# Optimization experiments

Measured on AMD Instinct MI355X. Metric: run time of the kernel, lower is better.

## Reference

```python
import jax, jax.numpy as jnp
import numpy as np

N = 50000   # nodes
D = 128     # feature / out_channels
E = 800000  # edges per edge type
L = 2       # num_layers
T = 2       # num edge types


def setup_inputs() -> dict:
    key = jax.random.key(0)
    ks = jax.random.split(key, 6)
    x = jax.random.normal(ks[0], (N, D), dtype=jnp.float32)
    h = jax.random.normal(ks[1], (N, D), dtype=jnp.float32)  # unused by forward, kept for fidelity
    edge_index_a = jax.random.randint(ks[2], (2, E), 0, N)
    edge_index_b = jax.random.randint(ks[3], (2, E), 0, N)
    Wl = (jax.random.normal(ks[4], (L, T, D, D), dtype=jnp.float32) * 0.05)
    bl = jnp.zeros((L, T, D), dtype=jnp.float32)
    Wr = (jax.random.normal(ks[5], (L, T, D, D), dtype=jnp.float32) * 0.05)
    return {"x": x, "h": h, "edge_index_a": edge_index_a, "edge_index_b": edge_index_b,
            "Wl": Wl, "bl": bl, "Wr": Wr}


def _sage(x, edge_index, Wl, bl, Wr):
    # PyG SAGEConv: lin_l(mean_{j->i} x_j) + lin_r(x_i); lin_l has bias, lin_r does not.
    src, dst = edge_index[0], edge_index[1]
    msg_sum = jax.ops.segment_sum(x[src], dst, num_segments=N)            # [N, D]
    deg = jax.ops.segment_sum(jnp.ones((edge_index.shape[1],), x.dtype), dst, num_segments=N)
    mean = msg_sum / jnp.maximum(deg, 1.0)[:, None]
    return mean @ Wl + bl + x @ Wr


def reference(x, h, edge_index_a, edge_index_b, Wl, bl, Wr):
    out = x
    for l in range(L):
        # HeteroConv default aggregation: sum over edge types with same dst node type
        out = (_sage(out, edge_index_a, Wl[l, 0], bl[l, 0], Wr[l, 0])
               + _sage(out, edge_index_b, Wl[l, 1], bl[l, 1], Wr[l, 1]))
    return jax.nn.sigmoid(out)
```

## Files before the change

### kernel.cpp

```cpp
#include <hip/hip_runtime.h>
#include <math.h>

#define N_NODES 50000
#define D 128
#define NE 800000
#define BN 64
#define NBUCK 782
#define CAP 1280
#define EPB 4096
#define PBLK 196
#define F2B_BLKS 6250
#define WPREP_BLKS 384
#define MPITCH 68

typedef unsigned int uint;
typedef unsigned short ushort;
typedef unsigned char uchar;

using bf16x8 = __attribute__((ext_vector_type(8))) short;
using f32x4  = __attribute__((ext_vector_type(4))) float;

__device__ __forceinline__ float bflo(uint w) {
    union { uint u; float f; } c; c.u = w << 16; return c.f;
}
__device__ __forceinline__ float bfhi(uint w) {
    union { uint u; float f; } c; c.u = w & 0xffff0000u; return c.f;
}
__device__ __forceinline__ uint fp2bf_rn(float f) {
    union { float f; uint u; } c; c.f = f;
    return (c.u + 0x7fffu + ((c.u >> 16) & 1u)) >> 16;
}

__global__ __launch_bounds__(256) void build_kernel(
    const float4* __restrict__ x4, uint2* __restrict__ featb2,
    uint* __restrict__ feat8w,
    const float* __restrict__ Wl, const float* __restrict__ Wr,
    ushort* __restrict__ Wpack,
    const int* __restrict__ srcA, const int* __restrict__ dstA,
    const int* __restrict__ srcB, const int* __restrict__ dstB,
    int* __restrict__ bcurA, int* __restrict__ bcurB,
    uint* __restrict__ ebufA, uint* __restrict__ ebufB) {
    const int blk = blockIdx.x;
    const int t   = threadIdx.x;
    if (blk < 2 * PBLK) {
        __shared__ int h[NBUCK];
        __shared__ int base[NBUCK];
        const int typ = blk >= PBLK;
        const int* src = typ ? srcB : srcA;
        const int* dst = typ ? dstB : dstA;
        int* bc        = typ ? bcurB : bcurA;
        uint* ebuf     = typ ? ebufB : ebufA;
        const int e0 = (blk - (typ ? PBLK : 0)) * EPB;
        for (int j = t; j < NBUCK; j += 256) h[j] = 0;
        __syncthreads();
#pragma unroll
        for (int i = 0; i < EPB / 256; ++i) {
            const int e = e0 + t + i * 256;
            if (e < NE) atomicAdd(&h[dst[e] >> 6], 1);
        }
        __syncthreads();
        for (int j = t; j < NBUCK; j += 256) {
            const int c = h[j];
            base[j] = c ? atomicAdd(&bc[j], c) : 0;
            h[j] = 0;
        }
        __syncthreads();
#pragma unroll
        for (int i = 0; i < EPB / 256; ++i) {
            const int e = e0 + t + i * 256;
            if (e < NE) {
                const int d  = dst[e];
                const int bk = d >> 6;
                const int pos = atomicAdd(&h[bk], 1);
                const int off = base[bk] + pos;
                if (off < CAP)
                    ebuf[(size_t)bk * CAP + off] = (uint)src[e] | ((uint)(d & 63) << 17);
            }
        }
    } else if (blk < 2 * PBLK + F2B_BLKS) {
        const int i = (blk - 2 * PBLK) * 256 + t;
        float4 v = x4[i];
        uint2 o;
        o.x = fp2bf_rn(v.x) | (fp2bf_rn(v.y) << 16);
        o.y = fp2bf_rn(v.z) | (fp2bf_rn(v.w) << 16);
        featb2[i] = o;
        int pk = __builtin_amdgcn_cvt_pk_fp8_f32(v.x, v.y, 0, false);
        pk = __builtin_amdgcn_cvt_pk_fp8_f32(v.z, v.w, pk, true);
        feat8w[i] = (uint)pk;
    } else {
        const int i   = (blk - 2 * PBLK - F2B_BLKS) * 256 + t;
        const int l   = i / 49152;
        const int rem = i % 49152;
        const int ks  = rem / 4096;
        const int n   = (rem % 4096) / 32;
        const int kk  = rem % 32;
        const int r   = ks * 32 + kk;
        float v;
        if (r < 128)       v = Wl[(((size_t)l * 2 + 0) * 128 + r) * 128 + n];
        else if (r < 256)  v = Wl[(((size_t)l * 2 + 1) * 128 + (r - 128)) * 128 + n];
        else               v = Wr[(((size_t)l * 2 + 0) * 128 + (r - 256)) * 128 + n]
                             + Wr[(((size_t)l * 2 + 1) * 128 + (r - 256)) * 128 + n];
        Wpack[i] = (ushort)fp2bf_rn(v);
    }
}

__global__ __launch_bounds__(256) void csrfill_kernel(
    const uint* __restrict__ ebufA, const uint* __restrict__ ebufB,
    const int* __restrict__ bcntA, const int* __restrict__ bcntB,
    ushort* __restrict__ lidxA, ushort* __restrict__ lidxB,
    int* __restrict__ pbeg, int* __restrict__ pdeg, uchar* __restrict__ ord) {
    __shared__ uint rlds[2][CAP];
    __shared__ int cnt[128], ex[128], cur[128];
    const int b = blockIdx.x;
    const int t = threadIdx.x;

    if (t < 128) cnt[t] = 0;
    int countA = bcntA[b]; if (countA > CAP) countA = CAP;
    int countB = bcntB[b]; if (countB > CAP) countB = CAP;
    const uint* ebA = ebufA + (size_t)b * CAP;
    const uint* ebB = ebufB + (size_t)b * CAP;
    for (int e = t; e < countA; e += 256) rlds[0][e] = ebA[e];
    for (int e = t; e < countB; e += 256) rlds[1][e] = ebB[e];
    __syncthreads();
    for (int e = t; e < countA; e += 256) atomicAdd(&cnt[rlds[0][e] >> 17], 1);
    for (int e = t; e < countB; e += 256) atomicAdd(&cnt[64 + (rlds[1][e] >> 17)], 1);
    __syncthreads();
    if (t < 128) ex[t] = cnt[t];
    __syncthreads();
    for (int off = 1; off < 64; off <<= 1) {
        int v = 0;
        if (t < 128 && (t & 63) >= off) v = ex[t - off];
        __syncthreads();
        if (t < 128 && (t & 63) >= off) ex[t] += v;
        __syncthreads();
    }
    if (t < 128) {
        ex[t] -= cnt[t];
        cur[t] = ex[t];
        const int node = b * BN + (t & 63);
        if (node < N_NODES) {
            const int base = (t >> 6) * N_NODES;
            pbeg[base + node] = b * CAP + ex[t];
            pdeg[base + node] = cnt[t];
        }
        const int li = cnt[t];
        int r = 0;
#pragma unroll 8
        for (int j = 0; j < 128; ++j) {
            const int lj = cnt[j];
            r += (lj > li) || (lj == li && j < t);
        }
        ord[b * 128 + r] = (uchar)t;
    }
    __syncthreads();
    for (int e = t; e < countA; e += 256) {
        const uint rec = rlds[0][e];
        const int p = atomicAdd(&cur[rec >> 17], 1);
        lidxA[(size_t)b * CAP + p] = (ushort)(rec & 0x1FFFFu);
    }
    for (int e = t; e < countB; e += 256) {
        const uint rec = rlds[1][e];
        const int p = atomicAdd(&cur[64 + (rec >> 17)], 1);
        lidxB[(size_t)b * CAP + p] = (ushort)(rec & 0x1FFFFu);
    }
}

__global__ __launch_bounds__(1024, 8) void fused_kernel(
    const uint4* __restrict__ feat,
    const uint4* __restrict__ feat8,
    const ushort* __restrict__ lidxA, const ushort* __restrict__ lidxB,
    const int* __restrict__ pbeg, const int* __restrict__ pdeg,
    const uchar* __restrict__ ord,
    const ushort* __restrict__ Wpack,
    const float* __restrict__ bias0, const float* __restrict__ bias1,
    float* __restrict__ outf, ushort* __restrict__ outb,
    uchar* __restrict__ out8, int act) {

    __shared__ uint   mlds[2 * BN * MPITCH];
    __shared__ ushort slidx[2][CAP];
    __shared__ int    lbeg[128], ldeg[128];
    __shared__ uchar  lslot[128];

    const int b = blockIdx.x;
    const int t = threadIdx.x;

    {
        const uint* gA = (const uint*)(lidxA + (size_t)b * CAP);
        const uint* gB = (const uint*)(lidxB + (size_t)b * CAP);
        uint* sA = (uint*)slidx[0];
        uint* sB = (uint*)slidx[1];
        for (int i = t; i < CAP / 2; i += 1024) sA[i] = gA[i];
        for (int i = t; i < CAP / 2; i += 1024) sB[i] = gB[i];
    }
    if (t < 128) {
        const int slot = (int)ord[b * 128 + t];
        lslot[t] = (uchar)slot;
        const int node = b * BN + (slot & 63);
        int bg = 0, dg = 0;
        if (node < N_NODES) {
            const int base = (slot >> 6) * N_NODES;
            bg = pbeg[base + node] - b * CAP;
            dg = pdeg[base + node];
        }
        lbeg[t] = bg; ldeg[t] = dg;
    }
    __syncthreads();

    const int j = t >> 3, ln = t & 7;
    {
        const int slot = (int)lslot[j];
        const int typ = slot >> 6, lnode = slot & 63;
        const int beg = lbeg[j], deg = ldeg[j];
        const ushort* lx = slidx[typ] + beg;
        float a[16] = {0.f,0.f,0.f,0.f,0.f,0.f,0.f,0.f,
                       0.f,0.f,0.f,0.f,0.f,0.f,0.f,0.f};
#define ACC16(vv) { \
    auto q0 = __builtin_amdgcn_cvt_pk_f32_fp8((int)(vv).x, false); \
    auto q1 = __builtin_amdgcn_cvt_pk_f32_fp8((int)(vv).x, true);  \
    a[0]+=q0[0];  a[1]+=q0[1];  a[2]+=q1[0];  a[3]+=q1[1];         \
    auto q2 = __builtin_amdgcn_cvt_pk_f32_fp8((int)(vv).y, false); \
    auto q3 = __builtin_amdgcn_cvt_pk_f32_fp8((int)(vv).y, true);  \
    a[4]+=q2[0];  a[5]+=q2[1];  a[6]+=q3[0];  a[7]+=q3[1];         \
    auto q4 = __builtin_amdgcn_cvt_pk_f32_fp8((int)(vv).z, false); \
    auto q5 = __builtin_amdgcn_cvt_pk_f32_fp8((int)(vv).z, true);  \
    a[8]+=q4[0];  a[9]+=q4[1];  a[10]+=q5[0]; a[11]+=q5[1];        \
    auto q6 = __builtin_amdgcn_cvt_pk_f32_fp8((int)(vv).w, false); \
    auto q7 = __builtin_amdgcn_cvt_pk_f32_fp8((int)(vv).w, true);  \
    a[12]+=q6[0]; a[13]+=q6[1]; a[14]+=q7[0]; a[15]+=q7[1]; }
        int e = 0;
        for (; e + 2 <= deg; e += 2) {
            uint4 w0 = feat8[(size_t)lx[e]     * 8 + ln];
            uint4 w1 = feat8[(size_t)lx[e + 1] * 8 + ln];
            ACC16(w0);
            ACC16(w1);
        }
        if (e < deg) {
            uint4 w0 = feat8[(size_t)lx[e] * 8 + ln];
            ACC16(w0);
        }
#undef ACC16
        const float invd = 1.0f / fmaxf((float)deg, 1.0f);
        uint4 o0, o1;
        o0.x = fp2bf_rn(a[0] * invd)  | (fp2bf_rn(a[1] * invd)  << 16);
        o0.y = fp2bf_rn(a[2] * invd)  | (fp2bf_rn(a[3] * invd)  << 16);
        o0.z = fp2bf_rn(a[4] * invd)  | (fp2bf_rn(a[5] * invd)  << 16);
        o0.w = fp2bf_rn(a[6] * invd)  | (fp2bf_rn(a[7] * invd)  << 16);
        o1.x = fp2bf_rn(a[8] * invd)  | (fp2bf_rn(a[9] * invd)  << 16);
        o1.y = fp2bf_rn(a[10] * invd) | (fp2bf_rn(a[11] * invd) << 16);
        o1.z = fp2bf_rn(a[12] * invd) | (fp2bf_rn(a[13] * invd) << 16);
        o1.w = fp2bf_rn(a[14] * invd) | (fp2bf_rn(a[15] * invd) << 16);
        uint4* mp = reinterpret_cast<uint4*>(&mlds[(typ * BN + lnode) * MPITCH + ln * 8]);
        mp[0] = o0;
        mp[1] = o1;
    }
    __syncthreads();

    const int wid = t >> 6, wl = t & 63;
    const int mrow = wl & 15, g = wl >> 4;
    const int mt   = wid >> 2;
    const int ntp  = (wid & 3) * 2;
    const int arow = mt * 16 + mrow;

    f32x4 acc0 = (f32x4){0.f, 0.f, 0.f, 0.f};
    f32x4 acc1 = (f32x4){0.f, 0.f, 0.f, 0.f};
#pragma unroll
    for (int ks = 0; ks < 12; ++ks) {
        union { uint4 u; bf16x8 v; } av;
        if (ks < 8) {
            av.u = *reinterpret_cast<const uint4*>(
                &mlds[((ks >> 2) * BN + arow) * MPITCH + (ks & 3) * 16 + g * 4]);
        } else {
            int srow = b * BN + arow;
            if (srow >= N_NODES) srow = N_NODES - 1;
            av.u = feat[(size_t)srow * 16 + (ks & 3) * 4 + g];
        }
        const ushort* Wk = Wpack + (size_t)ks * 128 * 32;
        union { uint4 u; bf16x8 v; } bv0, bv1;
        bv0.u = *reinterpret_cast<const uint4*>(Wk + ((ntp * 16 + mrow) * 32 + g * 8));
        bv1.u = *reinterpret_cast<const uint4*>(Wk + (((ntp + 1) * 16 + mrow) * 32 + g * 8));
        acc0 = __builtin_amdgcn_mfma_f32_16x16x32_bf16(av.v, bv0.v, acc0, 0, 0, 0);
        acc1 = __builtin_amdgcn_mfma_f32_16x16x32_bf16(av.v, bv1.v, acc1, 0, 0, 0);
    }

#pragma unroll
    for (int q = 0; q < 2; ++q) {
        const f32x4 av = q ? acc1 : acc0;
        const int col = (ntp + q) * 16 + mrow;
        const float bias = bias0[col] + bias1[col];
#pragma unroll
        for (int r = 0; r < 4; ++r) {
            const int row = b * BN + mt * 16 + g * 4 + r;
            if (row < N_NODES) {
                const float v = av[r] + bias;
                if (act) {
                    outf[(size_t)row * D + col] = 1.0f / (1.0f + expf(-v));
                } else {
                    outb[(size_t)row * D + col] = (ushort)fp2bf_rn(v);
                    const int pk = __builtin_amdgcn_cvt_pk_fp8_f32(v, v, 0, false);
                    out8[(size_t)row * D + col] = (uchar)(pk & 0xFF);
                }
            }
        }
    }
}

extern "C" void kernel_launch(void* const* d_in, const int* in_sizes, int n_in,
                              void* d_out, int out_size, void* d_ws, size_t ws_size,
                              hipStream_t stream) {
    const float* x    = (const float*)d_in[0];
    const int*   ei_a = (const int*)d_in[2];
    const int*   ei_b = (const int*)d_in[3];
    const float* Wl   = (const float*)d_in[4];
    const float* bl   = (const float*)d_in[5];
    const float* Wr   = (const float*)d_in[6];
    float* out = (float*)d_out;

    ushort* featb = (ushort*)d_ws;
    ushort* feat2 = featb + (size_t)N_NODES * D;
    uchar* feat8  = (uchar*)(feat2 + (size_t)N_NODES * D);
    uchar* feat28 = feat8 + (size_t)N_NODES * D;
    uint* ebufA = (uint*)(feat28 + (size_t)N_NODES * D);
    uint* ebufB = ebufA + (size_t)NBUCK * CAP;
    ushort* lidxA = (ushort*)(ebufB + (size_t)NBUCK * CAP);
    ushort* lidxB = lidxA + (size_t)NBUCK * CAP;
    int* pbeg  = (int*)(lidxB + (size_t)NBUCK * CAP);
    int* pdeg  = pbeg + 2 * N_NODES;
    uchar* ord = (uchar*)(pdeg + 2 * N_NODES);
    int* bcurA = (int*)(((size_t)(ord + NBUCK * 128) + 15) & ~(size_t)15);
    int* bcurB = bcurA + NBUCK;
    ushort* Wpack = (ushort*)(((size_t)(bcurB + NBUCK) + 63) & ~(size_t)63);

    const int* srcA = ei_a;
    const int* dstA = ei_a + NE;
    const int* srcB = ei_b;
    const int* dstB = ei_b + NE;

    hipMemsetAsync(bcurA, 0, 2ull * NBUCK * sizeof(int), stream);
    build_kernel<<<2 * PBLK + F2B_BLKS + WPREP_BLKS, 256, 0, stream>>>(
        (const float4*)x, (uint2*)featb, (uint*)feat8, Wl, Wr, Wpack,
        srcA, dstA, srcB, dstB, bcurA, bcurB, ebufA, ebufB);
    csrfill_kernel<<<NBUCK, 256, 0, stream>>>(
        ebufA, ebufB, bcurA, bcurB, lidxA, lidxB, pbeg, pdeg, ord);

    fused_kernel<<<NBUCK, 1024, 0, stream>>>(
        (const uint4*)featb, (const uint4*)feat8, lidxA, lidxB, pbeg, pdeg, ord,
        Wpack, bl + 0 * D, bl + 1 * D, nullptr, feat2, feat28, 0);
    fused_kernel<<<NBUCK, 1024, 0, stream>>>(
        (const uint4*)feat2, (const uint4*)feat28, lidxA, lidxB, pbeg, pdeg, ord,
        Wpack + (size_t)12 * 128 * 32, bl + 2 * D, bl + 3 * D, out, nullptr, nullptr, 1);
}
```

Measured before the change: 167.0 us.

## Fuse CSR fill into first layer kernel and pack per-node metadata

Removes the separate csrfill kernel and performs the per-bucket counting sort inside the first fused layer kernel, with mlds serving as scratch for the raw edge records. The sorted local indices and a packed begin/degree/slot word per node go to global memory so the second layer can reload them instead of re-sorting. The gather loop is unrolled to four edges. An extra barrier is added before the mean is written into mlds, since that buffer now also holds the sort scratch. This saves one launch and the pbeg/pdeg/ord indirection, but the sort now runs inside 1024-thread blocks where most threads sit idle.

```diff
diff --git a/kernel.cpp b/kernel.cpp
--- a/kernel.cpp
+++ b/kernel.cpp
@@ -104,113 +104,96 @@
     }
 }
 
-__global__ __launch_bounds__(256) void csrfill_kernel(
-    const uint* __restrict__ ebufA, const uint* __restrict__ ebufB,
-    const int* __restrict__ bcntA, const int* __restrict__ bcntB,
-    ushort* __restrict__ lidxA, ushort* __restrict__ lidxB,
-    int* __restrict__ pbeg, int* __restrict__ pdeg, uchar* __restrict__ ord) {
-    __shared__ uint rlds[2][CAP];
-    __shared__ int cnt[128], ex[128], cur[128];
-    const int b = blockIdx.x;
-    const int t = threadIdx.x;
-
-    if (t < 128) cnt[t] = 0;
-    int countA = bcntA[b]; if (countA > CAP) countA = CAP;
-    int countB = bcntB[b]; if (countB > CAP) countB = CAP;
-    const uint* ebA = ebufA + (size_t)b * CAP;
-    const uint* ebB = ebufB + (size_t)b * CAP;
-    for (int e = t; e < countA; e += 256) rlds[0][e] = ebA[e];
-    for (int e = t; e < countB; e += 256) rlds[1][e] = ebB[e];
-    __syncthreads();
-    for (int e = t; e < countA; e += 256) atomicAdd(&cnt[rlds[0][e] >> 17], 1);
-    for (int e = t; e < countB; e += 256) atomicAdd(&cnt[64 + (rlds[1][e] >> 17)], 1);
-    __syncthreads();
-    if (t < 128) ex[t] = cnt[t];
-    __syncthreads();
-    for (int off = 1; off < 64; off <<= 1) {
-        int v = 0;
-        if (t < 128 && (t & 63) >= off) v = ex[t - off];
-        __syncthreads();
-        if (t < 128 && (t & 63) >= off) ex[t] += v;
-        __syncthreads();
-    }
-    if (t < 128) {
-        ex[t] -= cnt[t];
-        cur[t] = ex[t];
-        const int node = b * BN + (t & 63);
-        if (node < N_NODES) {
-            const int base = (t >> 6) * N_NODES;
-            pbeg[base + node] = b * CAP + ex[t];
-            pdeg[base + node] = cnt[t];
-        }
-        const int li = cnt[t];
-        int r = 0;
-#pragma unroll 8
-        for (int j = 0; j < 128; ++j) {
-            const int lj = cnt[j];
-            r += (lj > li) || (lj == li && j < t);
-        }
-        ord[b * 128 + r] = (uchar)t;
-    }
-    __syncthreads();
-    for (int e = t; e < countA; e += 256) {
-        const uint rec = rlds[0][e];
-        const int p = atomicAdd(&cur[rec >> 17], 1);
-        lidxA[(size_t)b * CAP + p] = (ushort)(rec & 0x1FFFFu);
-    }
-    for (int e = t; e < countB; e += 256) {
-        const uint rec = rlds[1][e];
-        const int p = atomicAdd(&cur[64 + (rec >> 17)], 1);
-        lidxB[(size_t)b * CAP + p] = (ushort)(rec & 0x1FFFFu);
-    }
-}
-
 __global__ __launch_bounds__(1024, 8) void fused_kernel(
     const uint4* __restrict__ feat,
     const uint4* __restrict__ feat8,
-    const ushort* __restrict__ lidxA, const ushort* __restrict__ lidxB,
-    const int* __restrict__ pbeg, const int* __restrict__ pdeg,
-    const uchar* __restrict__ ord,
+    const uint* __restrict__ ebufA, const uint* __restrict__ ebufB,
+    const int* __restrict__ bcntA, const int* __restrict__ bcntB,
+    uint* __restrict__ glidx,
+    uint* __restrict__ gmeta,
     const ushort* __restrict__ Wpack,
     const float* __restrict__ bias0, const float* __restrict__ bias1,
     float* __restrict__ outf, ushort* __restrict__ outb,
-    uchar* __restrict__ out8, int act) {
+    uchar* __restrict__ out8, int sort, int act) {
 
     __shared__ uint   mlds[2 * BN * MPITCH];
     __shared__ ushort slidx[2][CAP];
-    __shared__ int    lbeg[128], ldeg[128];
-    __shared__ uchar  lslot[128];
+    __shared__ uint   lmeta[128];
+    __shared__ int    cnt[128], ex[128], cur[128];
 
     const int b = blockIdx.x;
     const int t = threadIdx.x;
-
-    {
-        const uint* gA = (const uint*)(lidxA + (size_t)b * CAP);
-        const uint* gB = (const uint*)(lidxB + (size_t)b * CAP);
+    uint* gl = glidx + (size_t)b * CAP;
+
+    if (sort) {
+        if (t < 128) cnt[t] = 0;
+        int countA = bcntA[b]; if (countA > CAP) countA = CAP;
+        int countB = bcntB[b]; if (countB > CAP) countB = CAP;
+        const uint* ebA = ebufA + (size_t)b * CAP;
+        const uint* ebB = ebufB + (size_t)b * CAP;
+        for (int e = t; e < countA; e += 1024) mlds[e] = ebA[e];
+        for (int e = t; e < countB; e += 1024) mlds[CAP + e] = ebB[e];
+        __syncthreads();
+        for (int e = t; e < countA; e += 1024) atomicAdd(&cnt[mlds[e] >> 17], 1);
+        for (int e = t; e < countB; e += 1024) atomicAdd(&cnt[64 + (mlds[CAP + e] >> 17)], 1);
+        __syncthreads();
+        if (t < 128) ex[t] = cnt[t];
+        __syncthreads();
+        for (int off = 1; off < 64; off <<= 1) {
+            int v = 0;
+            if (t < 128 && (t & 63) >= off) v = ex[t - off];
+            __syncthreads();
+            if (t < 128 && (t & 63) >= off) ex[t] += v;
+            __syncthreads();
+        }
+        if (t < 128) {
+            ex[t] -= cnt[t];
+            cur[t] = ex[t];
+            const int li = cnt[t];
+            int r = 0;
+#pragma unroll 8
+            for (int j = 0; j < 128; ++j) {
+                const int lj = cnt[j];
+                r += (lj > li) || (lj == li && j < t);
+            }
+            const uint m = (uint)ex[t] | ((uint)cnt[t] << 11) | ((uint)t << 22);
+            lmeta[r] = m;
+            gmeta[b * 128 + r] = m;
+        }
+        __syncthreads();
+        for (int e = t; e < countA; e += 1024) {
+            const uint rec = mlds[e];
+            const int p = atomicAdd(&cur[rec >> 17], 1);
+            slidx[0][p] = (ushort)(rec & 0x1FFFFu);
+        }
+        for (int e = t; e < countB; e += 1024) {
+            const uint rec = mlds[CAP + e];
+            const int p = atomicAdd(&cur[64 + (rec >> 17)], 1);
+            slidx[1][p] = (ushort)(rec & 0x1FFFFu);
+        }
+        __syncthreads();
+        {
+            const uint* sA = (const uint*)slidx[0];
+            const uint* sB = (const uint*)slidx[1];
+            for (int i = t; i < CAP / 2; i += 1024) gl[i] = sA[i];
+            for (int i = t; i < CAP / 2; i += 1024) gl[CAP / 2 + i] = sB[i];
+        }
+    } else {
         uint* sA = (uint*)slidx[0];
         uint* sB = (uint*)slidx[1];
-        for (int i = t; i < CAP / 2; i += 1024) sA[i] = gA[i];
-        for (int i = t; i < CAP / 2; i += 1024) sB[i] = gB[i];
-    }
-    if (t < 128) {
-        const int slot = (int)ord[b * 128 + t];
-        lslot[t] = (uchar)slot;
-        const int node = b * BN + (slot & 63);
-        int bg = 0, dg = 0;
-        if (node < N_NODES) {
-            const int base = (slot >> 6) * N_NODES;
-            bg = pbeg[base + node] - b * CAP;
-            dg = pdeg[base + node];
-        }
-        lbeg[t] = bg; ldeg[t] = dg;
-    }
-    __syncthreads();
+        for (int i = t; i < CAP / 2; i += 1024) sA[i] = gl[i];
+        for (int i = t; i < CAP / 2; i += 1024) sB[i] = gl[CAP / 2 + i];
+        if (t < 128) lmeta[t] = gmeta[b * 128 + t];
+        __syncthreads();
+    }
 
     const int j = t >> 3, ln = t & 7;
     {
-        const int slot = (int)lslot[j];
+        const uint m = lmeta[j];
+        const int beg = (int)(m & 0x7FFu);
+        const int deg = (int)((m >> 11) & 0x7FFu);
+        const int slot = (int)(m >> 22);
         const int typ = slot >> 6, lnode = slot & 63;
-        const int beg = lbeg[j], deg = ldeg[j];
         const ushort* lx = slidx[typ] + beg;
         float a[16] = {0.f,0.f,0.f,0.f,0.f,0.f,0.f,0.f,
                        0.f,0.f,0.f,0.f,0.f,0.f,0.f,0.f};
@@ -228,17 +211,19 @@
     auto q7 = __builtin_amdgcn_cvt_pk_f32_fp8((int)(vv).w, true);  \
     a[12]+=q6[0]; a[13]+=q6[1]; a[14]+=q7[0]; a[15]+=q7[1]; }
         int e = 0;
-        for (; e + 2 <= deg; e += 2) {
+        for (; e + 4 <= deg; e += 4) {
             uint4 w0 = feat8[(size_t)lx[e]     * 8 + ln];
             uint4 w1 = feat8[(size_t)lx[e + 1] * 8 + ln];
-            ACC16(w0);
-            ACC16(w1);
-        }
-        if (e < deg) {
+            uint4 w2 = feat8[(size_t)lx[e + 2] * 8 + ln];
+            uint4 w3 = feat8[(size_t)lx[e + 3] * 8 + ln];
+            ACC16(w0); ACC16(w1); ACC16(w2); ACC16(w3);
+        }
+        for (; e < deg; ++e) {
             uint4 w0 = feat8[(size_t)lx[e] * 8 + ln];
             ACC16(w0);
         }
 #undef ACC16
+        __syncthreads();
         const float invd = 1.0f / fmaxf((float)deg, 1.0f);
         uint4 o0, o1;
         o0.x = fp2bf_rn(a[0] * invd)  | (fp2bf_rn(a[1] * invd)  << 16);
@@ -321,13 +306,10 @@
     uchar* feat28 = feat8 + (size_t)N_NODES * D;
     uint* ebufA = (uint*)(feat28 + (size_t)N_NODES * D);
     uint* ebufB = ebufA + (size_t)NBUCK * CAP;
-    ushort* lidxA = (ushort*)(ebufB + (size_t)NBUCK * CAP);
-    ushort* lidxB = lidxA + (size_t)NBUCK * CAP;
-    int* pbeg  = (int*)(lidxB + (size_t)NBUCK * CAP);
-    int* pdeg  = pbeg + 2 * N_NODES;
-    uchar* ord = (uchar*)(pdeg + 2 * N_NODES);
-    int* bcurA = (int*)(((size_t)(ord + NBUCK * 128) + 15) & ~(size_t)15);
-    int* bcurB = bcurA + NBUCK;
+    uint* glidx = ebufB + (size_t)NBUCK * CAP;
+    uint* gmeta = glidx + (size_t)NBUCK * CAP;
+    int* bcurA  = (int*)(gmeta + (size_t)NBUCK * 128);
+    int* bcurB  = bcurA + NBUCK;
     ushort* Wpack = (ushort*)(((size_t)(bcurB + NBUCK) + 63) & ~(size_t)63);
 
     const int* srcA = ei_a;
@@ -339,13 +321,13 @@
     build_kernel<<<2 * PBLK + F2B_BLKS + WPREP_BLKS, 256, 0, stream>>>(
         (const float4*)x, (uint2*)featb, (uint*)feat8, Wl, Wr, Wpack,
         srcA, dstA, srcB, dstB, bcurA, bcurB, ebufA, ebufB);
-    csrfill_kernel<<<NBUCK, 256, 0, stream>>>(
-        ebufA, ebufB, bcurA, bcurB, lidxA, lidxB, pbeg, pdeg, ord);
 
     fused_kernel<<<NBUCK, 1024, 0, stream>>>(
-        (const uint4*)featb, (const uint4*)feat8, lidxA, lidxB, pbeg, pdeg, ord,
-        Wpack, bl + 0 * D, bl + 1 * D, nullptr, feat2, feat28, 0);
+        (const uint4*)featb, (const uint4*)feat8, ebufA, ebufB, bcurA, bcurB,
+        glidx, gmeta, Wpack, bl + 0 * D, bl + 1 * D,
+        nullptr, feat2, feat28, 1, 0);
     fused_kernel<<<NBUCK, 1024, 0, stream>>>(
-        (const uint4*)feat2, (const uint4*)feat28, lidxA, lidxB, pbeg, pdeg, ord,
-        Wpack + (size_t)12 * 128 * 32, bl + 2 * D, bl + 3 * D, out, nullptr, nullptr, 1);
-}
+        (const uint4*)feat2, (const uint4*)feat28, ebufA, ebufB, bcurA, bcurB,
+        glidx, gmeta, Wpack + (size_t)12 * 128 * 32, bl + 2 * D, bl + 3 * D,
+        out, nullptr, nullptr, 0, 1);
+}
```

New measurement: 187.1 us. 1.12x slower.
